# Kernel optimization log

Measured on AMD Instinct MI355X. Metric: run time of the kernel, lower is better.

## Reference

```python
import jax, jax.numpy as jnp
import numpy as np

B, S, D_IN, D_Q, D_V, H = 2, 2048, 1024, 1024, 1024, 16
HD_Q, HD_V = D_Q // H, D_V // H
SCALE = float(D_Q) ** 0.5  # source scales by sqrt(d_q), NOT sqrt(head_dim)


def setup_inputs() -> dict:
    key = jax.random.key(0)
    k1, k2, k3, k4, k5 = jax.random.split(key, 5)
    return {
        "x": jax.random.normal(k1, (B, S, D_IN), dtype=jnp.float32),
        "w_q": jax.random.normal(k2, (D_IN, D_Q), dtype=jnp.float32),
        "w_k": jax.random.normal(k3, (D_IN, D_Q), dtype=jnp.float32),
        "w_v": jax.random.normal(k4, (D_IN, D_V), dtype=jnp.float32),
        "W_o": jax.random.normal(k5, (D_IN, D_V), dtype=jnp.float32),
    }


def reference(x, w_q, w_k, w_v, W_o):
    b, s, _ = x.shape
    # projections: [b, s, d]
    q = x @ w_q
    k = x @ w_k
    v = x @ w_v
    # split heads -> [b, h, s, hd]
    Q = q.reshape(b, s, H, HD_Q).transpose(0, 2, 1, 3)
    K = k.reshape(b, s, H, HD_Q).transpose(0, 2, 1, 3)
    V = v.reshape(b, s, H, HD_V).transpose(0, 2, 1, 3)
    # full [b, h, s, s] score matrix (naive attention, as in source)
    scores = jnp.einsum("bhqd,bhkd->bhqk", Q, K)
    # FAITHFUL QUIRK: source applies softmax over dim=0 (batch axis)
    attn = jax.nn.softmax(scores / SCALE, axis=0)
    vals = jnp.einsum("bhqk,bhkd->bhqd", attn, V)
    vals = vals.transpose(0, 2, 1, 3).reshape(b, s, D_V)
    return vals @ W_o
```

## Files before the change

kernel.cpp:

```cpp
#include <hip/hip_runtime.h>


typedef _Float16 f16;
typedef __attribute__((ext_vector_type(8))) _Float16 f16x8;
typedef __attribute__((ext_vector_type(4))) _Float16 f16x4;
typedef __attribute__((ext_vector_type(4))) float f32x4;
typedef __attribute__((ext_vector_type(16))) float f32x16;

#define MFMA16(a,b,c)  __builtin_amdgcn_mfma_f32_16x16x32_f16(a,b,c,0,0,0)
#define MFMA32(a,b,c)  __builtin_amdgcn_mfma_f32_32x32x16_f16(a,b,c,0,0,0)
#define GLD16(gp, lp) __builtin_amdgcn_global_load_lds(                         \
    (const __attribute__((address_space(1))) void*)(gp),                        \
    (__attribute__((address_space(3))) void*)(lp), 16, 0, 0)

__global__ __launch_bounds__(256) void prep(const float* __restrict__ x,
                                            const float* __restrict__ w0, const float* __restrict__ w1,
                                            const float* __restrict__ w2, const float* __restrict__ w3,
                                            f16* __restrict__ xh,
                                            f16* __restrict__ o0, f16* __restrict__ o1,
                                            f16* __restrict__ o2, f16* __restrict__ o3) {
    const int bb = blockIdx.x;
    const int tid = threadIdx.x;
    if (bb >= 1024) {
        int i = (bb - 1024) * 256 + tid;
        float4 v = ((const float4*)x)[i];
        f16x4 h;
        h[0] = (f16)v.x; h[1] = (f16)v.y; h[2] = (f16)v.z; h[3] = (f16)v.w;
        *(f16x4*)(xh + (long)i * 4) = h;
        return;
    }
    const float* w; f16* o;
    switch (bb & 3) {
        case 0: w = w0; o = o0; break;
        case 1: w = w1; o = o1; break;
        case 2: w = w2; o = o2; break;
        default: w = w3; o = o3; break;
    }
    __shared__ alignas(16) f16 t[64][72];
    const int d0 = ((bb >> 2) & 15) * 64, j0 = (bb >> 6) * 64;
    #pragma unroll
    for (int it = 0; it < 4; ++it) {
        int idx = it * 256 + tid;
        int row = idx >> 4, c4 = idx & 15;
        float4 v = *(const float4*)(w + (long)(d0 + row) * 1024 + j0 + c4 * 4);
        f16x4 h;
        h[0] = (f16)v.x; h[1] = (f16)v.y; h[2] = (f16)v.z; h[3] = (f16)v.w;
        *(f16x4*)&t[row][c4 * 4] = h;
    }
    __syncthreads();
    #pragma unroll
    for (int it = 0; it < 4; ++it) {
        int idx = it * 256 + tid;
        int jr = idx >> 4, d4 = idx & 15;
        f16x4 h;
        #pragma unroll
        for (int m = 0; m < 4; ++m) h[m] = t[d4 * 4 + m][jr];
        *(f16x4*)(o + (long)(j0 + jr) * 1024 + d0 + d4 * 4) = h;
    }
}

__global__ __launch_bounds__(256, 1) void gemm_qkv(const f16* __restrict__ A,
                                                   const f16* __restrict__ Wt,
                                                   f16* __restrict__ Qg,
                                                   f16* __restrict__ Kg,
                                                   f16* __restrict__ Vtg) {
    __shared__ alignas(16) f16 smem[16384];
    f16* As = smem;
    f16* Bs = smem + 8192;
    const int tid = threadIdx.x;
    const int wave = tid >> 6, lane = tid & 63;
    const int l15 = lane & 15, lq = lane >> 4;
    const int sw = l15 & 7;
    const int m0 = blockIdx.x * 128, n0 = blockIdx.y * 128;
    const int wr = (wave >> 1) * 64, wc = (wave & 1) * 64;
    const int r8 = lane >> 3;
    const int swc8 = ((lane & 7) ^ r8) * 8;

    f32x4 acc[4][4] = {};

    for (int kt = 0; kt < 16; ++kt) {
        __syncthreads();
        #pragma unroll
        for (int i = 0; i < 4; ++i) {
            GLD16(A  + (long)(m0 + wave * 32 + i * 8 + r8) * 1024 + kt * 64 + swc8, As + (wave * 32 + i * 8) * 64);
            GLD16(Wt + (long)(n0 + wave * 32 + i * 8 + r8) * 1024 + kt * 64 + swc8, Bs + (wave * 32 + i * 8) * 64);
        }
        __syncthreads();
        #pragma unroll
        for (int s2 = 0; s2 < 2; ++s2) {
            const int rc = ((s2 * 4 + lq) ^ sw) << 3;
            f16x8 af[4], bf[4];
            #pragma unroll
            for (int i = 0; i < 4; ++i) af[i] = *(const f16x8*)&As[(wr + i * 16 + l15) * 64 + rc];
            #pragma unroll
            for (int j = 0; j < 4; ++j) bf[j] = *(const f16x8*)&Bs[(wc + j * 16 + l15) * 64 + rc];
            #pragma unroll
            for (int i = 0; i < 4; ++i)
                #pragma unroll
                for (int j = 0; j < 4; ++j)
                    acc[i][j] = MFMA16(af[i], bf[j], acc[i][j]);
        }
    }

    const int sel = n0 >> 10;
    const int nb = n0 - (sel << 10);

    if (sel < 2) {
        f16* dst = sel == 0 ? Qg : Kg;
        const float qs = sel == 0 ? 0.045084219f : 1.0f;
        __syncthreads();
        #pragma unroll
        for (int i = 0; i < 4; ++i)
            #pragma unroll
            for (int j = 0; j < 4; ++j) {
                int row0 = wr + i * 16 + lq * 4;
                int colb = wc + j * 16 + l15;
                int chunk = colb >> 3, sub = colb & 7;
                #pragma unroll
                for (int r = 0; r < 4; ++r) {
                    int row = row0 + r;
                    smem[row * 128 + ((chunk ^ (row & 7)) << 3) + sub] = (f16)(acc[i][j][r] * qs);
                }
            }
        __syncthreads();
        #pragma unroll
        for (int e = 0; e < 8; ++e) {
            int id = e * 256 + tid;
            int row = id >> 4, c = id & 15;
            f16x8 v = *(const f16x8*)&smem[row * 128 + ((c ^ (row & 7)) << 3)];
            int gr = m0 + row, b = gr >> 11, s = gr & 2047;
            int gc = nb + c * 8, hh = gc >> 6, hd = gc & 63;
            *(f16x8*)(dst + (long)((b * 16 + hh) * 2048 + s) * 64 + hd) = v;
        }
    } else {
        #pragma unroll
        for (int i = 0; i < 4; ++i)
            #pragma unroll
            for (int j = 0; j < 4; ++j) {
                int gr0 = m0 + wr + i * 16 + lq * 4;
                int gc  = nb + wc + j * 16 + l15;
                int b = gr0 >> 11, s = gr0 & 2047;
                int hh = gc >> 6, hd = gc & 63;
                f16x4 v;
                #pragma unroll
                for (int r = 0; r < 4; ++r) v[r] = (f16)acc[i][j][r];
                *(f16x4*)(Vtg + (long)((b * 16 + hh) * 64 + hd) * 2048 + s) = v;
            }
    }
}

template<int NSUM>
__global__ __launch_bounds__(256, 1) void gemm_out(const f16* __restrict__ A0,
                                                   const f16* __restrict__ A1,
                                                   const f16* __restrict__ A2,
                                                   const f16* __restrict__ A3,
                                                   const f16* __restrict__ Bt,
                                                   float* __restrict__ outp) {
    __shared__ alignas(16) f16 As[64][72];
    __shared__ alignas(16) f16 Bs[128][64];
    const int tid = threadIdx.x;
    const int wave = tid >> 6, lane = tid & 63;
    const int l15 = lane & 15, lq = lane >> 4;
    const int sw = l15 & 7;
    const int m0 = blockIdx.x * 64, n0 = blockIdx.y * 128;
    const int wr = (wave >> 1) * 32, wc = (wave & 1) * 64;
    const int r8 = lane >> 3;
    const int swc8 = ((lane & 7) ^ r8) * 8;

    f32x4 acc[2][4] = {};

    for (int kt = 0; kt < 16; ++kt) {
        __syncthreads();
        #pragma unroll
        for (int it = 0; it < 2; ++it) {
            int idx = it * 256 + tid;
            int row = idx >> 3, c = idx & 7;
            long off = (long)(m0 + row) * 1024 + kt * 64 + c * 8;
            f16x8 a = *(const f16x8*)(A0 + off) + *(const f16x8*)(A1 + off);
            if constexpr (NSUM == 4)
                a = a + *(const f16x8*)(A2 + off) + *(const f16x8*)(A3 + off);
            *(f16x8*)&As[row][c * 8] = a;
        }
        #pragma unroll
        for (int i = 0; i < 4; ++i)
            GLD16(Bt + (long)(n0 + wave * 32 + i * 8 + r8) * 1024 + kt * 64 + swc8, &Bs[wave * 32 + i * 8][0]);
        __syncthreads();
        #pragma unroll
        for (int s2 = 0; s2 < 2; ++s2) {
            const int rc = ((s2 * 4 + lq) ^ sw) << 3;
            f16x8 af[2], bf[4];
            #pragma unroll
            for (int i = 0; i < 2; ++i) af[i] = *(const f16x8*)&As[wr + i * 16 + l15][s2 * 32 + lq * 8];
            #pragma unroll
            for (int j = 0; j < 4; ++j) bf[j] = *(const f16x8*)&Bs[wc + j * 16 + l15][rc];
            #pragma unroll
            for (int i = 0; i < 2; ++i)
                #pragma unroll
                for (int j = 0; j < 4; ++j)
                    acc[i][j] = MFMA16(af[i], bf[j], acc[i][j]);
        }
    }

    #pragma unroll
    for (int i = 0; i < 2; ++i)
        #pragma unroll
        for (int j = 0; j < 4; ++j) {
            int gr0 = m0 + wr + i * 16 + lq * 4;
            int gc  = n0 + wc + j * 16 + l15;
            #pragma unroll
            for (int r = 0; r < 4; ++r)
                outp[(long)(gr0 + r) * 1024 + gc] = acc[i][j][r];
        }
}

__global__ __launch_bounds__(256, 3) void attention_kernel(const f16* __restrict__ Qg,
                                                           const f16* __restrict__ Kg,
                                                           const f16* __restrict__ Vtg,
                                                           f16* __restrict__ v0,
                                                           f16* __restrict__ v1,
                                                           f16* __restrict__ v2,
                                                           f16* __restrict__ v3) {
    __shared__ alignas(16) f16 Ks [2][2][32][64];
    __shared__ alignas(16) f16 Vts[2][2][64][32];
    const int tid = threadIdx.x;
    const int wave = tid >> 6, lane = tid & 63;
    const int l31 = lane & 31, hi = lane >> 5;
    const int kchunk = l31 & 7;
    const int vcb = (l31 >> 1) & 3;

    const int NS = gridDim.x >> 8;
    const int nt = 64 / NS;
    const int bid = blockIdx.x;
    const int xcd = bid & 7, sl = bid >> 3;
    const int h  = xcd * 2 + (sl & 1);
    const int qt = (sl >> 1) & 15, ks = sl >> 5;
    const int q0 = qt * 128;
    const int key0 = ks * (nt << 5);
    f16* vals = ks == 0 ? v0 : ks == 1 ? v1 : ks == 2 ? v2 : v3;
    const int qr = q0 + wave * 32;

    f16x8 qfr[2][4];
    #pragma unroll
    for (int b2 = 0; b2 < 2; ++b2)
        #pragma unroll
        for (int s2 = 0; s2 < 4; ++s2)
            qfr[b2][s2] = *(const f16x8*)(Qg + (long)((b2 * 16 + h) * 2048 + qr + l31) * 64
                                          + s2 * 16 + hi * 8);

    f32x16 acc[2][2] = {};

    const int tb = wave & 1;
    const int r8 = lane >> 3;
    const int swc8 = ((lane & 7) ^ r8) * 8;
    const f16* kbase = Kg  + (long)((tb * 16 + h) * 2048 + key0) * 64 + r8 * 64 + swc8;
    const f16* vbase = Vtg + (long)((tb * 16 + h) * 64 + (lane >> 2)) * 2048 + key0
                       + ((lane & 3) ^ ((lane >> 3) & 3)) * 8;

    auto stage = [&](int kt, int buf) {
        if (wave < 2) {
            const f16* g = kbase + kt * 2048;
            f16* l = &Ks[buf][tb][0][0];
            #pragma unroll
            for (int i = 0; i < 4; ++i) GLD16(g + i * 512, l + i * 512);
        } else {
            const f16* g = vbase + kt * 32;
            f16* l = &Vts[buf][tb][0][0];
            #pragma unroll
            for (int i = 0; i < 4; ++i) GLD16(g + (long)i * 16 * 2048, l + i * 512);
        }
    };

    const f16* VtsF = &Vts[0][0][0][0];
    const f16x8 ones8 = {(f16)1.f,(f16)1.f,(f16)1.f,(f16)1.f,(f16)1.f,(f16)1.f,(f16)1.f,(f16)1.f};

    stage(0, 0);
    for (int kt = 0; kt < nt; ++kt) {
        const int cur = kt & 1;
        __syncthreads();
        if (kt < nt - 1) stage(kt + 1, cur ^ 1);

        f32x16 S0 = {}, S1 = {};
        __builtin_amdgcn_s_setprio(1);
        #pragma unroll
        for (int s2 = 0; s2 < 4; ++s2) {
            const int rc = ((s2 * 2 + hi) ^ kchunk) << 3;
            f16x8 a0 = *(const f16x8*)&Ks[cur][0][l31][rc];
            f16x8 a1 = *(const f16x8*)&Ks[cur][1][l31][rc];
            S0 = MFMA32(a0, qfr[0][s2], S0);
            S1 = MFMA32(a1, qfr[1][s2], S1);
        }
        __builtin_amdgcn_s_setprio(0);

        unsigned pk[8];
        #pragma unroll
        for (int p = 0; p < 8; ++p) {
            float e0 = __builtin_amdgcn_exp2f(S1[2 * p]     - S0[2 * p]);
            float e1 = __builtin_amdgcn_exp2f(S1[2 * p + 1] - S0[2 * p + 1]);
            float pa = __builtin_amdgcn_rcpf(1.0f + e0);
            float pb = __builtin_amdgcn_rcpf(1.0f + e1);
            auto h2 = __builtin_amdgcn_cvt_pkrtz(pa, pb);
            pk[p] = __builtin_bit_cast(unsigned, h2);
        }

        f16x8 pf0[2], pf1[2];
        #pragma unroll
        for (int keyh = 0; keyh < 2; ++keyh) {
            unsigned a0 = pk[4 * keyh + 0], b0 = pk[4 * keyh + 2];
            unsigned a1 = pk[4 * keyh + 1], b1 = pk[4 * keyh + 3];
            asm("v_permlane32_swap_b32 %0, %1" : "+v"(a0), "+v"(b0));
            asm("v_permlane32_swap_b32 %0, %1" : "+v"(a1), "+v"(b1));
            union { unsigned u[4]; f16x8 v; } m;
            m.u[0] = a0; m.u[1] = a1; m.u[2] = b0; m.u[3] = b1;
            pf0[keyh] = m.v;
            pf1[keyh] = ones8 - m.v;
        }

        __builtin_amdgcn_s_setprio(1);
        #pragma unroll
        for (int pb = 0; pb < 2; ++pb)
            #pragma unroll
            for (int keyh = 0; keyh < 2; ++keyh) {
                const f16x8 pfr = pb ? pf1[keyh] : pf0[keyh];
                #pragma unroll
                for (int hdh = 0; hdh < 2; ++hdh) {
                    f16x8 vf = *(const f16x8*)&VtsF[cur * 4096 + pb * 2048 + hdh * 1024
                                                    + l31 * 32 + (((keyh * 2 + hi) ^ vcb) << 3)];
                    acc[pb][hdh] = MFMA32(vf, pfr, acc[pb][hdh]);
                }
            }
        __builtin_amdgcn_s_setprio(0);
    }

    #pragma unroll
    for (int pb = 0; pb < 2; ++pb)
        #pragma unroll
        for (int hdh = 0; hdh < 2; ++hdh)
            #pragma unroll
            for (int g = 0; g < 4; ++g) {
                f16x4 ov;
                #pragma unroll
                for (int r2 = 0; r2 < 4; ++r2) ov[r2] = (f16)acc[pb][hdh][g * 4 + r2];
                *(f16x4*)(vals + (long)(pb * 2048 + qr + l31) * 1024
                          + h * 64 + hdh * 32 + g * 8 + hi * 4) = ov;
            }
}

extern "C" void kernel_launch(void* const* d_in, const int* in_sizes, int n_in,
                              void* d_out, int out_size, void* d_ws, size_t ws_size,
                              hipStream_t stream) {
    const float* x  = (const float*)d_in[0];
    const float* wq = (const float*)d_in[1];
    const float* wk = (const float*)d_in[2];
    const float* wv = (const float*)d_in[3];
    const float* wo = (const float*)d_in[4];

    char* ws = (char*)d_ws;
    f16* xh    = (f16*)(ws);
    f16* wqT   = (f16*)(ws + 8388608);
    f16* wkT   = (f16*)(ws + 10485760);
    f16* wvT   = (f16*)(ws + 12582912);
    f16* woT   = (f16*)(ws + 14680064);
    f16* Qg    = (f16*)(ws + 16777216);
    f16* Kg    = (f16*)(ws + 25165824);
    f16* Vtg   = (f16*)(ws + 33554432);
    f16* vals1 = (f16*)(ws + 41943040);
    f16* vals2 = (f16*)(ws + 50331648);
    f16* vals3 = (f16*)(ws + 58720256);
    f16* vals0 = xh;
    (void)in_sizes; (void)n_in; (void)out_size;

    const int NS = (ws_size >= (size_t)67108864) ? 4 : 2;

    prep<<<5120, 256, 0, stream>>>(x, wq, wk, wv, wo, xh, wqT, wkT, wvT, woT);

    gemm_qkv<<<dim3(32, 24), 256, 0, stream>>>(xh, wqT, Qg, Kg, Vtg);

    attention_kernel<<<NS * 256, 256, 0, stream>>>(Qg, Kg, Vtg, vals0, vals1, vals2, vals3);

    if (NS == 4)
        gemm_out<4><<<dim3(64, 8), 256, 0, stream>>>(vals0, vals1, vals2, vals3, woT, (float*)d_out);
    else
        gemm_out<2><<<dim3(64, 8), 256, 0, stream>>>(vals0, vals1, vals0, vals0, woT, (float*)d_out);
}
```

Baseline: 194.0 us.

## Triple-buffer attention K/V staging and split keys three ways

The attention kernel now keeps three LDS buffers for K and V tiles and prefetches two tiles ahead. It uses explicit vmcnt waits plus a raw barrier in place of a full syncthreads per iteration. The key-dimension split drops from four to three partial-value buffers, with uneven tile counts across splits, and the output GEMM sums three partials instead of four. The aim is to hide global-load latency and cut partial-sum traffic, at the cost of more LDS per block (possibly lower occupancy), fewer blocks (768 vs 1024), and some load imbalance.

```diff
diff --git a/kernel.cpp b/kernel.cpp
--- a/kernel.cpp
+++ b/kernel.cpp
@@ -177,8 +177,8 @@
             int row = idx >> 3, c = idx & 7;
             long off = (long)(m0 + row) * 1024 + kt * 64 + c * 8;
             f16x8 a = *(const f16x8*)(A0 + off) + *(const f16x8*)(A1 + off);
-            if constexpr (NSUM == 4)
-                a = a + *(const f16x8*)(A2 + off) + *(const f16x8*)(A3 + off);
+            if constexpr (NSUM >= 3) a = a + *(const f16x8*)(A2 + off);
+            if constexpr (NSUM >= 4) a = a + *(const f16x8*)(A3 + off);
             *(f16x8*)&As[row][c * 8] = a;
         }
         #pragma unroll
@@ -218,10 +218,9 @@
                                                            const f16* __restrict__ Vtg,
                                                            f16* __restrict__ v0,
                                                            f16* __restrict__ v1,
-                                                           f16* __restrict__ v2,
-                                                           f16* __restrict__ v3) {
-    __shared__ alignas(16) f16 Ks [2][2][32][64];
-    __shared__ alignas(16) f16 Vts[2][2][64][32];
+                                                           f16* __restrict__ v2) {
+    __shared__ alignas(16) f16 Ks [3][2][32][64];
+    __shared__ alignas(16) f16 Vts[3][2][64][32];
     const int tid = threadIdx.x;
     const int wave = tid >> 6, lane = tid & 63;
     const int l31 = lane & 31, hi = lane >> 5;
@@ -229,14 +228,16 @@
     const int vcb = (l31 >> 1) & 3;
 
     const int NS = gridDim.x >> 8;
-    const int nt = 64 / NS;
     const int bid = blockIdx.x;
     const int xcd = bid & 7, sl = bid >> 3;
     const int h  = xcd * 2 + (sl & 1);
     const int qt = (sl >> 1) & 15, ks = sl >> 5;
     const int q0 = qt * 128;
-    const int key0 = ks * (nt << 5);
-    f16* vals = ks == 0 ? v0 : ks == 1 ? v1 : ks == 2 ? v2 : v3;
+    const int kb = 64 / NS, krem = 64 % NS;
+    const int nt = kb + (ks < krem ? 1 : 0);
+    const int ts0 = ks * kb + (ks < krem ? ks : krem);
+    const int key0 = ts0 * 32;
+    f16* vals = ks == 0 ? v0 : ks == 1 ? v1 : v2;
     const int qr = q0 + wave * 32;
 
     f16x8 qfr[2][4];
@@ -274,10 +275,14 @@
     const f16x8 ones8 = {(f16)1.f,(f16)1.f,(f16)1.f,(f16)1.f,(f16)1.f,(f16)1.f,(f16)1.f,(f16)1.f};
 
     stage(0, 0);
+    stage(1, 1);
+    int cur = 0, nx2 = 2;
     for (int kt = 0; kt < nt; ++kt) {
-        const int cur = kt & 1;
-        __syncthreads();
-        if (kt < nt - 1) stage(kt + 1, cur ^ 1);
+        if (kt == nt - 1) asm volatile("s_waitcnt vmcnt(0)" ::: "memory");
+        else              asm volatile("s_waitcnt vmcnt(4)" ::: "memory");
+        __builtin_amdgcn_s_barrier();
+        __builtin_amdgcn_sched_barrier(0);
+        if (kt + 2 < nt) stage(kt + 2, nx2);
 
         f32x16 S0 = {}, S1 = {};
         __builtin_amdgcn_s_setprio(1);
@@ -329,6 +334,9 @@
                 }
             }
         __builtin_amdgcn_s_setprio(0);
+
+        cur = cur == 2 ? 0 : cur + 1;
+        nx2 = nx2 == 2 ? 0 : nx2 + 1;
     }
 
     #pragma unroll
@@ -365,20 +373,19 @@
     f16* Vtg   = (f16*)(ws + 33554432);
     f16* vals1 = (f16*)(ws + 41943040);
     f16* vals2 = (f16*)(ws + 50331648);
-    f16* vals3 = (f16*)(ws + 58720256);
     f16* vals0 = xh;
     (void)in_sizes; (void)n_in; (void)out_size;
 
-    const int NS = (ws_size >= (size_t)67108864) ? 4 : 2;
+    const int NS = (ws_size >= (size_t)58720256) ? 3 : 2;
 
     prep<<<5120, 256, 0, stream>>>(x, wq, wk, wv, wo, xh, wqT, wkT, wvT, woT);
 
     gemm_qkv<<<dim3(32, 24), 256, 0, stream>>>(xh, wqT, Qg, Kg, Vtg);
 
-    attention_kernel<<<NS * 256, 256, 0, stream>>>(Qg, Kg, Vtg, vals0, vals1, vals2, vals3);
-
-    if (NS == 4)
-        gemm_out<4><<<dim3(64, 8), 256, 0, stream>>>(vals0, vals1, vals2, vals3, woT, (float*)d_out);
+    attention_kernel<<<NS * 256, 256, 0, stream>>>(Qg, Kg, Vtg, vals0, vals1, vals2);
+
+    if (NS == 3)
+        gemm_out<3><<<dim3(64, 8), 256, 0, stream>>>(vals0, vals1, vals2, vals0, woT, (float*)d_out);
     else
         gemm_out<2><<<dim3(64, 8), 256, 0, stream>>>(vals0, vals1, vals0, vals0, woT, (float*)d_out);
 }
```

New measurement: 192.9 us. Within noise of the previous version (-0.6%).
